# Performance work log

Measured on AMD Instinct MI355X. Metric: run time of the kernel, lower is better.

The kernel has to match this reference:

```python
import jax, jax.numpy as jnp
import numpy as np

NUM_GROUPS = 32
EPS = 1e-5


def setup_inputs() -> dict:
    key = jax.random.key(0)
    ks = jax.random.split(key, 6)
    B, C, H, W = 8, 128, 64, 64
    d = C // 8
    x = jax.random.normal(ks[0], (B, C, H, W), dtype=jnp.float32)
    # conv 1x1 weights stored as [out_ch, in_ch]; scaled like torch kaiming-uniform-ish
    s = 1.0 / np.sqrt(C)
    return {
        "x": x,
        "gn_w": jnp.ones((C,), jnp.float32),
        "gn_b": jnp.zeros((C,), jnp.float32),
        "q_w": jax.random.normal(ks[1], (d, C), jnp.float32) * s,
        "q_b": jnp.zeros((d,), jnp.float32),
        "k_w": jax.random.normal(ks[2], (d, C), jnp.float32) * s,
        "k_b": jnp.zeros((d,), jnp.float32),
        "v_w": jax.random.normal(ks[3], (C, C), jnp.float32) * s,
        "v_b": jnp.zeros((C,), jnp.float32),
        "p_w": jax.random.normal(ks[4], (C, C), jnp.float32) * s,
        "p_b": jnp.zeros((C,), jnp.float32),
    }


def _group_norm(x, w, b):
    B, C, H, W = x.shape
    g = NUM_GROUPS
    xr = x.reshape(B, g, C // g, H, W)
    mu = xr.mean(axis=(2, 3, 4), keepdims=True)
    var = xr.var(axis=(2, 3, 4), keepdims=True)
    xn = ((xr - mu) * jax.lax.rsqrt(var + EPS)).reshape(B, C, H, W)
    return xn * w[None, :, None, None] + b[None, :, None, None]


def reference(x, gn_w, gn_b, q_w, q_b, k_w, k_b, v_w, v_b, p_w, p_b):
    B, C, H, W = x.shape
    N = H * W
    h_ = _group_norm(x, gn_w, gn_b)            # [B,C,H,W]
    hf = h_.reshape(B, C, N)                   # flatten spatial
    # 1x1 convs == channel matmuls
    q = jnp.einsum('dc,bcn->bnd', q_w, hf) + q_b[None, None, :]   # [B,N,d]
    k = jnp.einsum('dc,bcn->bnd', k_w, hf) + k_b[None, None, :]   # [B,N,d]
    v = jnp.einsum('ec,bcn->ben', v_w, hf) + v_b[None, :, None]   # [B,C,N]
    d = q.shape[-1]
    scale = jnp.asarray(int(d) ** (-0.5), x.dtype)
    attn = jnp.einsum('bid,bjd->bij', q, k) * scale               # [B,N,N]
    attn = jax.nn.softmax(attn, axis=-1)
    a = jnp.einsum('bcj,bij->bci', v, attn)                       # [B,C,N]
    proj = jnp.einsum('ec,bcn->ben', p_w, a) + p_b[None, :, None]
    return x + proj.reshape(B, C, H, W)
```

## Files before the change

kernel.cpp:

```cpp
#include <hip/hip_runtime.h>
#include <math.h>


typedef short v8s __attribute__((ext_vector_type(8)));
typedef float v16f __attribute__((ext_vector_type(16)));

__device__ __forceinline__ unsigned short f2bf_rne(float f) {
  unsigned u = __float_as_uint(f);
  u += 0x7fffu + ((u >> 16) & 1u);
  return (unsigned short)(u >> 16);
}

__device__ __forceinline__ v8s mk8(unsigned a, unsigned b, unsigned c, unsigned d) {
  union { unsigned u[4]; v8s s; } x;
  x.u[0] = a; x.u[1] = b; x.u[2] = c; x.u[3] = d;
  return x.s;
}

__device__ __forceinline__ unsigned pack_trunc(float hi, float lo) {
  return __builtin_amdgcn_perm(__float_as_uint(hi), __float_as_uint(lo), 0x07060302u);
}

#define VT(b, n, c) (((((size_t)(b) * 256 + ((n) >> 4)) << 7) + (c)) * 16 + ((n) & 15))

#define WSB_MURS   0u
#define WSB_WCATB  4096u
#define WSB_BCAT   49152u
#define WSB_PWB    65536u
#define WSB_QBF    131072u
#define WSB_KBF    1310720u
#define WSB_VBF    2621440u

__global__ __launch_bounds__(512)
void gnprep_kernel(const float* __restrict__ x, float* __restrict__ mu_rs,
                   const float* __restrict__ qw, const float* __restrict__ qb,
                   const float* __restrict__ kw, const float* __restrict__ kb,
                   const float* __restrict__ vw, const float* __restrict__ vb,
                   const float* __restrict__ pw,
                   unsigned short* __restrict__ wcatb, float* __restrict__ bcat,
                   unsigned short* __restrict__ pwb) {
  const int id = blockIdx.x;
  {
    const float qs = 0.36067376022224085f;
    int idx = id * 512 + threadIdx.x;
    if (idx < 160 * 128) {
      int o = idx >> 7, c = idx & 127;
      float val;
      if (o < 16)       val = qw[o * 128 + c] * qs;
      else if (o < 32)  val = kw[(o - 16) * 128 + c];
      else              val = vw[(o - 32) * 128 + c];
      wcatb[idx] = f2bf_rne(val);
    } else if (idx < 160 * 128 + 160) {
      int o = idx - 160 * 128;
      bcat[o] = (o < 16) ? qb[o] * qs : (o < 32) ? kb[o - 16] : vb[o - 32];
    } else if (idx < 160 * 128 + 160 + 128 * 128) {
      int j = idx - (160 * 128 + 160);
      pwb[j] = f2bf_rne(pw[j]);
    }
  }
  const int bg = (id & 7) * 32 + (id >> 3);
  const float4* xp = (const float4*)(x + (size_t)bg * 16384);
  float s = 0.f, ss = 0.f;
#pragma unroll
  for (int u = 0; u < 8; ++u) {
    int i = threadIdx.x + u * 512;
    float4 v = xp[i];
    s  += v.x + v.y + v.z + v.w;
    ss += v.x * v.x + v.y * v.y + v.z * v.z + v.w * v.w;
  }
  for (int off = 32; off > 0; off >>= 1) {
    s  += __shfl_down(s, off, 64);
    ss += __shfl_down(ss, off, 64);
  }
  __shared__ float red[16];
  int lane = threadIdx.x & 63, wid = threadIdx.x >> 6;
  if (lane == 0) { red[wid * 2] = s; red[wid * 2 + 1] = ss; }
  __syncthreads();
  if (threadIdx.x == 0) {
    float S = 0.f, SS = 0.f;
    for (int w = 0; w < 8; ++w) { S += red[w * 2]; SS += red[w * 2 + 1]; }
    float mu  = S * (1.0f / 16384.0f);
    float var = SS * (1.0f / 16384.0f) - mu * mu;
    float rs  = rsqrtf(var + 1e-5f);
    mu_rs[bg * 2]     = mu;
    mu_rs[bg * 2 + 1] = rs;
  }
}

__global__ __launch_bounds__(512)
void qkv_kernel(const float* __restrict__ x, const float* __restrict__ gnw,
                const float* __restrict__ gnb, const float* __restrict__ mu_rs,
                const unsigned short* __restrict__ wcatb, const float* __restrict__ bcat,
                unsigned short* __restrict__ qTb, unsigned short* __restrict__ kbf,
                unsigned short* __restrict__ vbf) {
  __shared__ float scs[128], shs[128], bsh[160];
  const int id = blockIdx.x;
  const int b = id & 7, nb = (id >> 3) << 6;
  const int t = threadIdx.x;
  const int w = t >> 6, lane = t & 63, h = lane >> 5, l = lane & 31;
  const int nsub = w & 1, og = w >> 1;
  if (t < 128) {
    float mu = mu_rs[(b * 32 + (t >> 2)) * 2];
    float rs = mu_rs[(b * 32 + (t >> 2)) * 2 + 1];
    float gw = gnw[t], gb = gnb[t];
    scs[t] = rs * gw; shs[t] = gb - mu * rs * gw;
  }
  if (t < 160) bsh[t] = bcat[t];
  __syncthreads();

  const int n = nb + nsub * 32 + l;
  const float* xb = x + ((size_t)b * 128 << 12);
  const int otbase = (og == 0) ? 0 : og + 1;

  float xv[64];
#pragma unroll
  for (int ks = 0; ks < 8; ++ks)
#pragma unroll
    for (int p = 0; p < 8; ++p)
      xv[ks * 8 + p] = xb[((size_t)(ks * 16 + 8 * h + p) << 12) + n];

  v16f acc[2];
#pragma unroll
  for (int a2 = 0; a2 < 2; ++a2)
#pragma unroll
    for (int r = 0; r < 16; ++r) acc[a2][r] = 0.f;

#pragma unroll
  for (int ks = 0; ks < 8; ++ks) {
    const int c0 = ks * 16 + 8 * h;
    unsigned fd[4];
#pragma unroll
    for (int p = 0; p < 4; ++p) {
      int ca = c0 + 2 * p;
      float h0 = xv[ks * 8 + 2 * p]     * scs[ca]     + shs[ca];
      float h1 = xv[ks * 8 + 2 * p + 1] * scs[ca + 1] + shs[ca + 1];
      fd[p] = (unsigned)f2bf_rne(h0) | ((unsigned)f2bf_rne(h1) << 16);
    }
    v8s bf = mk8(fd[0], fd[1], fd[2], fd[3]);
    {
      v8s af = *(const v8s*)(wcatb + (otbase * 32 + l) * 128 + ks * 16 + 8 * h);
      acc[0] = __builtin_amdgcn_mfma_f32_32x32x16_bf16(af, bf, acc[0], 0, 0, 0);
    }
    if (og == 0) {
      v8s af = *(const v8s*)(wcatb + (32 + l) * 128 + ks * 16 + 8 * h);
      acc[1] = __builtin_amdgcn_mfma_f32_32x32x16_bf16(af, bf, acc[1], 0, 0, 0);
    }
  }

  if (og == 0) {
    const size_t nqk = ((size_t)b * 4096 + n) << 4;
#pragma unroll
    for (int r = 0; r < 16; ++r) {
      int o = 4 * h + (r & 3) + 8 * (r >> 2);
      unsigned short bv = f2bf_rne(acc[0][r] + bsh[o]);
      if (o < 16) qTb[((size_t)(b * 16 + o) << 12) + n] = bv;
      else        kbf[nqk + o - 16] = bv;
    }
#pragma unroll
    for (int r = 0; r < 16; ++r) {
      int o = 32 + 4 * h + (r & 3) + 8 * (r >> 2);
      vbf[VT(b, n, o - 32)] = f2bf_rne(acc[1][r] + bsh[o]);
    }
  } else {
#pragma unroll
    for (int r = 0; r < 16; ++r) {
      int o = otbase * 32 + 4 * h + (r & 3) + 8 * (r >> 2);
      vbf[VT(b, n, o - 32)] = f2bf_rne(acc[0][r] + bsh[o]);
    }
  }
}

#define VS 24
#define OTS 136

__global__ __launch_bounds__(256)
void attn_kernel(const unsigned short* __restrict__ qTb,
                 const unsigned short* __restrict__ kbf,
                 const unsigned short* __restrict__ vbf,
                 const unsigned short* __restrict__ pwb,
                 const float* __restrict__ pb,
                 const float* __restrict__ x,
                 float* __restrict__ out) {
  __shared__ alignas(16) unsigned short smem[2][512 * VS];
  __shared__ float l_lds[64];
  __shared__ float pbs[128];

  const int id = blockIdx.x;
  const int b = id & 7, i0 = (id >> 3) << 6;
  const int t = threadIdx.x;
  const int w = t >> 6, lane = t & 63, h = lane >> 5, l = lane & 31;
  const int jsub = w & 1, ihalf = w >> 1;

  const unsigned short* kg = kbf + ((size_t)b << 16);
  const unsigned short* vg = vbf + ((size_t)b << 19);

  if (t < 128) pbs[t] = pb[t];

  const int iglob = i0 + ihalf * 32 + l;
  unsigned qd[4];
#pragma unroll
  for (int e = 0; e < 4; ++e) {
    unsigned lo = qTb[((size_t)(b * 16 + 8 * h + 2 * e) << 12) + iglob];
    unsigned hi = qTb[((size_t)(b * 16 + 8 * h + 2 * e + 1) << 12) + iglob];
    qd[e] = lo | (hi << 16);
  }
  const v8s qf = mk8(qd[0], qd[1], qd[2], qd[3]);

  v16f zc;
#pragma unroll
  for (int r = 0; r < 16; ++r) zc[r] = 0.f;
  v16f acc[4];
#pragma unroll
  for (int ct = 0; ct < 4; ++ct)
#pragma unroll
    for (int r = 0; r < 16; ++r) acc[ct][r] = 0.f;
  float ls = 0.f;

  const int srow = w * 128 + (lane >> 1);
  const int sh16 = (lane & 1) * 8;

#pragma unroll
  for (int u = 0; u < 4; ++u) {
    v8s a = *(const v8s*)(vg + (size_t)(srow + 32 * u) * 16 + sh16);
    *(v8s*)(&smem[0][(srow + 32 * u) * VS + sh16]) = a;
  }
  if (t < 64) l_lds[t] = 0.f;
  __syncthreads();

  for (int tile = 0; tile < 64; ++tile) {
    const int tn = (tile + 1) & 63;
    unsigned short* const cur = smem[tile & 1];
    unsigned short* const nxt = smem[(tile + 1) & 1];

    v8s s[4];
#pragma unroll
    for (int u = 0; u < 4; ++u)
      s[u] = *(const v8s*)(vg + (size_t)tn * 8192 + (size_t)(srow + 32 * u) * 16 + sh16);

    v8s kf = *(const v8s*)(kg + (((size_t)(tile * 64 + jsub * 32 + l)) << 4) + 8 * h);

    v16f st = __builtin_amdgcn_mfma_f32_32x32x16_bf16(kf, qf, zc, 0, 0, 0);
    float pe[16];
#pragma unroll
    for (int r = 0; r < 16; ++r) { pe[r] = __builtin_amdgcn_exp2f(st[r]); ls += pe[r]; }
    unsigned G[8];
#pragma unroll
    for (int g = 0; g < 4; ++g) {
      G[2 * g]     = pack_trunc(pe[4 * g + 1], pe[4 * g]);
      G[2 * g + 1] = pack_trunc(pe[4 * g + 3], pe[4 * g + 2]);
    }
    unsigned S0 = h ? G[0] : G[2], S1 = h ? G[1] : G[3];
    unsigned S2 = h ? G[4] : G[6], S3 = h ? G[5] : G[7];
    unsigned R0 = (unsigned)__shfl_xor((int)S0, 32, 64);
    unsigned R1 = (unsigned)__shfl_xor((int)S1, 32, 64);
    unsigned R2 = (unsigned)__shfl_xor((int)S2, 32, 64);
    unsigned R3 = (unsigned)__shfl_xor((int)S3, 32, 64);
    v8s pf0 = h ? mk8(R0, R1, G[2], G[3]) : mk8(G[0], G[1], R0, R1);
    v8s pf1 = h ? mk8(R2, R3, G[6], G[7]) : mk8(G[4], G[5], R2, R3);

#pragma unroll
    for (int ct = 0; ct < 4; ++ct) {
      v8s vf0 = *(const v8s*)(&cur[((jsub * 2) * 128 + ct * 32 + l) * VS + 8 * h]);
      v8s vf1 = *(const v8s*)(&cur[((jsub * 2 + 1) * 128 + ct * 32 + l) * VS + 8 * h]);
      acc[ct] = __builtin_amdgcn_mfma_f32_32x32x16_bf16(vf0, pf0, acc[ct], 0, 0, 0);
      acc[ct] = __builtin_amdgcn_mfma_f32_32x32x16_bf16(vf1, pf1, acc[ct], 0, 0, 0);
    }

#pragma unroll
    for (int u = 0; u < 4; ++u)
      *(v8s*)(&nxt[(srow + 32 * u) * VS + sh16]) = s[u];

    __syncthreads();
  }

  atomicAdd(&l_lds[ihalf * 32 + l], ls);
  __syncthreads();

  float* const ov = (float*)smem;
  if (jsub == 1) {
#pragma unroll
    for (int ct = 0; ct < 4; ++ct)
#pragma unroll
      for (int q = 0; q < 4; ++q) {
        float4 v4 = {acc[ct][4 * q], acc[ct][4 * q + 1],
                     acc[ct][4 * q + 2], acc[ct][4 * q + 3]};
        *(float4*)&ov[((ct * 2 + ihalf) * 32 + l) * 36 + 4 * h + 8 * q] = v4;
      }
  }
  __syncthreads();
  if (jsub == 0) {
#pragma unroll
    for (int ct = 0; ct < 4; ++ct)
#pragma unroll
      for (int q = 0; q < 4; ++q) {
        float4 v4 = *(float4*)&ov[((ct * 2 + ihalf) * 32 + l) * 36 + 4 * h + 8 * q];
        acc[ct][4 * q]     += v4.x;
        acc[ct][4 * q + 1] += v4.y;
        acc[ct][4 * q + 2] += v4.z;
        acc[ct][4 * q + 3] += v4.w;
      }
  }
  __syncthreads();

  unsigned short* const oT = (unsigned short*)smem;
  if (jsub == 0) {
    const float li = 1.f / l_lds[ihalf * 32 + l];
    const int nrow = ihalf * 32 + l;
#pragma unroll
    for (int ct = 0; ct < 4; ++ct)
#pragma unroll
      for (int r = 0; r < 16; r += 2) {
        int c = ct * 32 + 4 * h + (r & 3) + 8 * (r >> 2);
        unsigned dw = (unsigned)f2bf_rne(acc[ct][r] * li) |
                      ((unsigned)f2bf_rne(acc[ct][r + 1] * li) << 16);
        *(unsigned*)(&oT[nrow * OTS + c]) = dw;
      }
  }
  __syncthreads();

#pragma unroll
  for (int nsub = 0; nsub < 2; ++nsub) {
    v16f a2;
#pragma unroll
    for (int r = 0; r < 16; ++r) a2[r] = 0.f;
#pragma unroll
    for (int ks = 0; ks < 8; ++ks) {
      v8s bf = *(const v8s*)(&oT[(nsub * 32 + l) * OTS + ks * 16 + 8 * h]);
      v8s af = *(const v8s*)(pwb + (w * 32 + l) * 128 + ks * 16 + 8 * h);
      a2 = __builtin_amdgcn_mfma_f32_32x32x16_bf16(af, bf, a2, 0, 0, 0);
    }
    const int n = i0 + nsub * 32 + l;
#pragma unroll
    for (int r = 0; r < 16; ++r) {
      int e = w * 32 + 4 * h + (r & 3) + 8 * (r >> 2);
      size_t idx = ((size_t)(b * 128 + e) << 12) + n;
      out[idx] = a2[r] + pbs[e] + x[idx];
    }
  }
}

extern "C" void kernel_launch(void* const* d_in, const int* in_sizes, int n_in,
                              void* d_out, int out_size, void* d_ws, size_t ws_size,
                              hipStream_t stream) {
  const float* x   = (const float*)d_in[0];
  const float* gnw = (const float*)d_in[1];
  const float* gnb = (const float*)d_in[2];
  const float* qw  = (const float*)d_in[3];
  const float* qb  = (const float*)d_in[4];
  const float* kw  = (const float*)d_in[5];
  const float* kb  = (const float*)d_in[6];
  const float* vw  = (const float*)d_in[7];
  const float* vb  = (const float*)d_in[8];
  const float* pw  = (const float*)d_in[9];
  const float* pb  = (const float*)d_in[10];
  float* out = (float*)d_out;
  char* ws = (char*)d_ws;

  float* mu_rs = (float*)(ws + WSB_MURS);
  unsigned short* wcatb = (unsigned short*)(ws + WSB_WCATB);
  float* bcat = (float*)(ws + WSB_BCAT);
  unsigned short* pwb = (unsigned short*)(ws + WSB_PWB);
  unsigned short* qTb = (unsigned short*)(ws + WSB_QBF);
  unsigned short* kbf = (unsigned short*)(ws + WSB_KBF);
  unsigned short* vbf = (unsigned short*)(ws + WSB_VBF);

  hipLaunchKernelGGL(gnprep_kernel, dim3(256), dim3(512), 0, stream,
                     x, mu_rs, qw, qb, kw, kb, vw, vb, pw, wcatb, bcat, pwb);
  hipLaunchKernelGGL(qkv_kernel, dim3(512), dim3(512), 0, stream,
                     x, gnw, gnb, mu_rs, wcatb, bcat, qTb, kbf, vbf);
  hipLaunchKernelGGL(attn_kernel, dim3(512), dim3(256), 0, stream,
                     qTb, kbf, vbf, pwb, pb, x, out);
}
```

Measured before the change: 163.5 us.

## Apply group norm in stats kernel and store bf16 tiled activations for QKV

The group-norm stats kernel now keeps its x tile in registers, applies the normalization and affine itself, and writes bf16 activations in an MFMA-friendly tiled layout to workspace. The QKV kernel then loads packed 8-element bf16 fragments directly instead of strided fp32 reads of x plus per-element normalization. This moves the strided fp32 read and conversion work out of the QKV stage and halves the bytes it reads. In exchange there is an extra 8 MB bf16 buffer round-trip through memory, and the stats kernel uses more registers.

Result: no change. 165.2 us (+1.0%).

```diff
diff --git a/kernel.cpp b/kernel.cpp
--- a/kernel.cpp
+++ b/kernel.cpp
@@ -22,23 +22,26 @@
 }
 
 #define VT(b, n, c) (((((size_t)(b) * 256 + ((n) >> 4)) << 7) + (c)) * 16 + ((n) & 15))
-
-#define WSB_MURS   0u
+#define XG(b, n, c) (((size_t)((b) * 256 + ((n) >> 4)) * 2048) + ((((c) >> 3)) << 7) + (((n) & 15) << 3) + ((c) & 7))
+
 #define WSB_WCATB  4096u
 #define WSB_BCAT   49152u
 #define WSB_PWB    65536u
 #define WSB_QBF    131072u
 #define WSB_KBF    1310720u
 #define WSB_VBF    2621440u
+#define WSB_XGN    11010048u
 
 __global__ __launch_bounds__(512)
-void gnprep_kernel(const float* __restrict__ x, float* __restrict__ mu_rs,
+void gnprep_kernel(const float* __restrict__ x,
+                   const float* __restrict__ gnw, const float* __restrict__ gnb,
                    const float* __restrict__ qw, const float* __restrict__ qb,
                    const float* __restrict__ kw, const float* __restrict__ kb,
                    const float* __restrict__ vw, const float* __restrict__ vb,
                    const float* __restrict__ pw,
                    unsigned short* __restrict__ wcatb, float* __restrict__ bcat,
-                   unsigned short* __restrict__ pwb) {
+                   unsigned short* __restrict__ pwb,
+                   unsigned short* __restrict__ xgn) {
   const int id = blockIdx.x;
   {
     const float qs = 0.36067376022224085f;
@@ -58,66 +61,86 @@
       pwb[j] = f2bf_rne(pw[j]);
     }
   }
-  const int bg = (id & 7) * 32 + (id >> 3);
+  const int b = id & 7, g = id >> 3;
+  const int bg = b * 32 + g;
   const float4* xp = (const float4*)(x + (size_t)bg * 16384);
+  float4 xv[8];
   float s = 0.f, ss = 0.f;
 #pragma unroll
   for (int u = 0; u < 8; ++u) {
-    int i = threadIdx.x + u * 512;
-    float4 v = xp[i];
-    s  += v.x + v.y + v.z + v.w;
-    ss += v.x * v.x + v.y * v.y + v.z * v.z + v.w * v.w;
+    xv[u] = xp[threadIdx.x + u * 512];
+    s  += xv[u].x + xv[u].y + xv[u].z + xv[u].w;
+    ss += xv[u].x * xv[u].x + xv[u].y * xv[u].y
+        + xv[u].z * xv[u].z + xv[u].w * xv[u].w;
   }
   for (int off = 32; off > 0; off >>= 1) {
     s  += __shfl_down(s, off, 64);
     ss += __shfl_down(ss, off, 64);
   }
   __shared__ float red[16];
+  __shared__ float musr[2];
   int lane = threadIdx.x & 63, wid = threadIdx.x >> 6;
   if (lane == 0) { red[wid * 2] = s; red[wid * 2 + 1] = ss; }
   __syncthreads();
   if (threadIdx.x == 0) {
     float S = 0.f, SS = 0.f;
-    for (int w = 0; w < 8; ++w) { S += red[w * 2]; SS += red[w * 2 + 1]; }
+    for (int w2 = 0; w2 < 8; ++w2) { S += red[w2 * 2]; SS += red[w2 * 2 + 1]; }
     float mu  = S * (1.0f / 16384.0f);
     float var = SS * (1.0f / 16384.0f) - mu * mu;
-    float rs  = rsqrtf(var + 1e-5f);
-    mu_rs[bg * 2]     = mu;
-    mu_rs[bg * 2 + 1] = rs;
+    musr[0] = mu;
+    musr[1] = rsqrtf(var + 1e-5f);
+  }
+  __syncthreads();
+  const float mu = musr[0], rs = musr[1];
+  float sc[4], sh[4];
+#pragma unroll
+  for (int cl = 0; cl < 4; ++cl) {
+    int c = 4 * g + cl;
+    sc[cl] = rs * gnw[c];
+    sh[cl] = gnb[c] - mu * sc[cl];
+  }
+#pragma unroll
+  for (int u = 0; u < 2; ++u) {
+    const int n0 = (threadIdx.x + u * 512) * 4;
+    const float* f0 = (const float*)&xv[u];
+    const float* f1 = (const float*)&xv[u + 2];
+    const float* f2 = (const float*)&xv[u + 4];
+    const float* f3 = (const float*)&xv[u + 6];
+#pragma unroll
+    for (int k = 0; k < 4; ++k) {
+      const int n = n0 + k;
+      unsigned e0 = f2bf_rne(f0[k] * sc[0] + sh[0]);
+      unsigned e1 = f2bf_rne(f1[k] * sc[1] + sh[1]);
+      unsigned e2 = f2bf_rne(f2[k] * sc[2] + sh[2]);
+      unsigned e3 = f2bf_rne(f3[k] * sc[3] + sh[3]);
+      uint2 uu; uu.x = e0 | (e1 << 16); uu.y = e2 | (e3 << 16);
+      *(uint2*)(xgn + XG(b, n, 4 * g)) = uu;
+    }
   }
 }
 
 __global__ __launch_bounds__(512)
-void qkv_kernel(const float* __restrict__ x, const float* __restrict__ gnw,
-                const float* __restrict__ gnb, const float* __restrict__ mu_rs,
+void qkv_kernel(const unsigned short* __restrict__ xgn,
                 const unsigned short* __restrict__ wcatb, const float* __restrict__ bcat,
                 unsigned short* __restrict__ qTb, unsigned short* __restrict__ kbf,
                 unsigned short* __restrict__ vbf) {
-  __shared__ float scs[128], shs[128], bsh[160];
+  __shared__ float bsh[160];
   const int id = blockIdx.x;
   const int b = id & 7, nb = (id >> 3) << 6;
   const int t = threadIdx.x;
   const int w = t >> 6, lane = t & 63, h = lane >> 5, l = lane & 31;
   const int nsub = w & 1, og = w >> 1;
-  if (t < 128) {
-    float mu = mu_rs[(b * 32 + (t >> 2)) * 2];
-    float rs = mu_rs[(b * 32 + (t >> 2)) * 2 + 1];
-    float gw = gnw[t], gb = gnb[t];
-    scs[t] = rs * gw; shs[t] = gb - mu * rs * gw;
-  }
   if (t < 160) bsh[t] = bcat[t];
   __syncthreads();
 
   const int n = nb + nsub * 32 + l;
-  const float* xb = x + ((size_t)b * 128 << 12);
   const int otbase = (og == 0) ? 0 : og + 1;
 
-  float xv[64];
+  const size_t xbase = (size_t)(b * 256 + (n >> 4)) * 2048 + ((n & 15) << 3);
+  v8s bf[8];
 #pragma unroll
   for (int ks = 0; ks < 8; ++ks)
-#pragma unroll
-    for (int p = 0; p < 8; ++p)
-      xv[ks * 8 + p] = xb[((size_t)(ks * 16 + 8 * h + p) << 12) + n];
+    bf[ks] = *(const v8s*)(xgn + xbase + ((ks * 2 + h) << 7));
 
   v16f acc[2];
 #pragma unroll
@@ -127,23 +150,13 @@
 
 #pragma unroll
   for (int ks = 0; ks < 8; ++ks) {
-    const int c0 = ks * 16 + 8 * h;
-    unsigned fd[4];
-#pragma unroll
-    for (int p = 0; p < 4; ++p) {
-      int ca = c0 + 2 * p;
-      float h0 = xv[ks * 8 + 2 * p]     * scs[ca]     + shs[ca];
-      float h1 = xv[ks * 8 + 2 * p + 1] * scs[ca + 1] + shs[ca + 1];
-      fd[p] = (unsigned)f2bf_rne(h0) | ((unsigned)f2bf_rne(h1) << 16);
-    }
-    v8s bf = mk8(fd[0], fd[1], fd[2], fd[3]);
     {
       v8s af = *(const v8s*)(wcatb + (otbase * 32 + l) * 128 + ks * 16 + 8 * h);
-      acc[0] = __builtin_amdgcn_mfma_f32_32x32x16_bf16(af, bf, acc[0], 0, 0, 0);
+      acc[0] = __builtin_amdgcn_mfma_f32_32x32x16_bf16(af, bf[ks], acc[0], 0, 0, 0);
     }
     if (og == 0) {
       v8s af = *(const v8s*)(wcatb + (32 + l) * 128 + ks * 16 + 8 * h);
-      acc[1] = __builtin_amdgcn_mfma_f32_32x32x16_bf16(af, bf, acc[1], 0, 0, 0);
+      acc[1] = __builtin_amdgcn_mfma_f32_32x32x16_bf16(af, bf[ks], acc[1], 0, 0, 0);
     }
   }
 
@@ -356,18 +369,18 @@
   float* out = (float*)d_out;
   char* ws = (char*)d_ws;
 
-  float* mu_rs = (float*)(ws + WSB_MURS);
   unsigned short* wcatb = (unsigned short*)(ws + WSB_WCATB);
   float* bcat = (float*)(ws + WSB_BCAT);
   unsigned short* pwb = (unsigned short*)(ws + WSB_PWB);
   unsigned short* qTb = (unsigned short*)(ws + WSB_QBF);
   unsigned short* kbf = (unsigned short*)(ws + WSB_KBF);
   unsigned short* vbf = (unsigned short*)(ws + WSB_VBF);
+  unsigned short* xgn = (unsigned short*)(ws + WSB_XGN);
 
   hipLaunchKernelGGL(gnprep_kernel, dim3(256), dim3(512), 0, stream,
-                     x, mu_rs, qw, qb, kw, kb, vw, vb, pw, wcatb, bcat, pwb);
+                     x, gnw, gnb, qw, qb, kw, kb, vw, vb, pw, wcatb, bcat, pwb, xgn);
   hipLaunchKernelGGL(qkv_kernel, dim3(512), dim3(512), 0, stream,
-                     x, gnw, gnb, mu_rs, wcatb, bcat, qTb, kbf, vbf);
+                     xgn, wcatb, bcat, qTb, kbf, vbf);
   hipLaunchKernelGGL(attn_kernel, dim3(512), dim3(256), 0, stream,
                      qTb, kbf, vbf, pwb, pb, x, out);
 }
```
